# Optimization experiments

Hardware: AMD Instinct MI355X
Metric: run time of the kernel (lower is better)

Reference implementation:

```python
import jax, jax.numpy as jnp
import numpy as np

STATE_DIM, SKILL_DIM = 256, 64
HID = 1024
LAT = 128
B = 4096
TEMP = 1.0


def _init_linear(key, fan_in, fan_out):
    # torch nn.Linear default init: U(-1/sqrt(fan_in), 1/sqrt(fan_in))
    kw, kb = jax.random.split(key)
    bound = 1.0 / np.sqrt(fan_in)
    W = jax.random.uniform(kw, (fan_in, fan_out), jnp.float32, -bound, bound)
    b = jax.random.uniform(kb, (fan_out,), jnp.float32, -bound, bound)
    return W, b


def setup_inputs() -> dict:
    key = jax.random.key(0)
    ks = jax.random.split(key, 8)
    x = jax.random.normal(ks[0], (B, STATE_DIM), jnp.float32)
    y = jax.random.normal(ks[1], (B, SKILL_DIM), jnp.float32)
    sW1, sb1 = _init_linear(ks[2], STATE_DIM, HID)
    sW2, sb2 = _init_linear(ks[3], HID, HID)
    sW3, sb3 = _init_linear(ks[4], HID, LAT)
    kW1, kb1 = _init_linear(ks[5], SKILL_DIM, HID)
    kW2, kb2 = _init_linear(ks[6], HID, HID)
    kW3, kb3 = _init_linear(ks[7], HID, LAT)
    return {
        "x": x, "y": y,
        "sW1": sW1, "sb1": sb1, "sW2": sW2, "sb2": sb2, "sW3": sW3, "sb3": sb3,
        "kW1": kW1, "kb1": kb1, "kW2": kW2, "kb2": kb2, "kW3": kW3, "kb3": kb3,
    }


def _mlp(x, W1, b1, W2, b2, W3, b3):
    h = jax.nn.relu(x @ W1 + b1)
    h = jax.nn.relu(h @ W2 + b2)
    return h @ W3 + b3


def _l2norm(v, eps=1e-12):
    # matches F.normalize(dim=-1): v / max(||v||, eps)
    n = jnp.sqrt(jnp.sum(v * v, axis=-1, keepdims=True))
    return v / jnp.maximum(n, eps)


def reference(x, y, sW1, sb1, sW2, sb2, sW3, sb3, kW1, kb1, kW2, kb2, kW3, kb3):
    zx = _l2norm(_mlp(x, sW1, sb1, sW2, sb2, sW3, sb3))  # [B, LAT]
    zy = _l2norm(_mlp(y, kW1, kb1, kW2, kb2, kW3, kb3))  # [B, LAT]
    # sum(x[:,None,:]*y[None,:,:], -1) == zx @ zy.T (same math, no BxBxD blowup)
    scores = jnp.einsum('id,jd->ij', zx, zy) / TEMP       # [B, B]
    # InfoNCE lower bound: log(B) - CE(scores, arange(B)), reduction='none'
    logp = jax.nn.log_softmax(scores, axis=-1)
    nll = jnp.diagonal(logp)                               # = -CE per row
    mi = jnp.log(jnp.float32(scores.shape[0])) + nll       # [B]
    return scores, mi
```

## Files before the change

kernel.cpp:

```cpp
#include <hip/hip_runtime.h>
#include <hip/hip_bf16.h>
#include <math.h>

typedef __bf16 v8bf __attribute__((ext_vector_type(8)));
typedef float  v4f  __attribute__((ext_vector_type(4)));

#define GPTR(p) ((const __attribute__((address_space(1))) void*)(p))
#define LPTR(p) ((__attribute__((address_space(3))) void*)(p))

__global__ __launch_bounds__(256)
void cast_xy_k(const float* __restrict__ x, const float* __restrict__ y,
               __hip_bfloat16* __restrict__ xb, __hip_bfloat16* __restrict__ yb,
               int nx4, int ntot4) {
    int i = blockIdx.x * 256 + threadIdx.x;
    if (i >= ntot4) return;
    const float* src; __hip_bfloat16* dst; int j;
    if (i < nx4) { src = x; dst = xb; j = i; }
    else         { src = y; dst = yb; j = i - nx4; }
    float4 v = ((const float4*)src)[j];
    __hip_bfloat16 h[4] = {__float2bfloat16(v.x), __float2bfloat16(v.y),
                           __float2bfloat16(v.z), __float2bfloat16(v.w)};
    ((short4*)dst)[j] = *(short4*)h;
}

struct TransAll {
    const float* src[6];
    __hip_bfloat16* dst[6];
    int K[6], N[6];
};

__global__ __launch_bounds__(256)
void transpose_all_k(TransAll a) {
    int w = blockIdx.z;
    int K = a.K[w], N = a.N[w];
    int kt = blockIdx.x * 32, nt = blockIdx.y * 32;
    if (kt >= K || nt >= N) return;
    __shared__ float t[32][33];
    int tx = threadIdx.x & 31, ty = threadIdx.x >> 5;
    const float* W = a.src[w];
    __hip_bfloat16* Wt = a.dst[w];
#pragma unroll
    for (int i = 0; i < 4; ++i)
        t[ty + i * 8][tx] = W[(size_t)(kt + ty + i * 8) * N + nt + tx];
    __syncthreads();
#pragma unroll
    for (int i = 0; i < 4; ++i)
        Wt[(size_t)(nt + ty + i * 8) * K + kt + tx] =
            __float2bfloat16(t[tx][ty + i * 8]);
}

__device__ __forceinline__ void gemm_mainloop(
    const __hip_bfloat16* __restrict__ A, const __hip_bfloat16* __restrict__ Bt,
    int lda, int ldb, int kbeg, int kend, int bm, int bn,
    int wid, int lane, int wr, int wc,
    __hip_bfloat16* As, __hip_bfloat16* Bs, v4f acc[4][4]) {
    const int crow = lane >> 3;
    const int ccol = (lane & 7) * 8;
    for (int k0 = kbeg; k0 < kend; k0 += 64) {
#pragma unroll
        for (int i = 0; i < 4; ++i) {
            int c = wid * 4 + i;
            __builtin_amdgcn_global_load_lds(
                GPTR(A + (size_t)(bm + c * 8 + crow) * lda + k0 + ccol),
                LPTR(As + c * 512), 16, 0, 0);
            __builtin_amdgcn_global_load_lds(
                GPTR(Bt + (size_t)(bn + c * 8 + crow) * ldb + k0 + ccol),
                LPTR(Bs + c * 512), 16, 0, 0);
        }
        __syncthreads();
#pragma unroll
        for (int kk = 0; kk < 64; kk += 32) {
            v8bf a[4], b[4];
#pragma unroll
            for (int i = 0; i < 4; ++i) {
                a[i] = *(const v8bf*)&As[(wr * 64 + i * 16 + (lane & 15)) * 64 + kk + (lane >> 4) * 8];
                b[i] = *(const v8bf*)&Bs[(wc * 64 + i * 16 + (lane & 15)) * 64 + kk + (lane >> 4) * 8];
            }
#pragma unroll
            for (int i = 0; i < 4; ++i)
#pragma unroll
                for (int j = 0; j < 4; ++j)
                    acc[i][j] = __builtin_amdgcn_mfma_f32_16x16x32_bf16(
                        a[i], b[j], acc[i][j], 0, 0, 0);
        }
        __syncthreads();
    }
}

struct MlpArgs {
    const __hip_bfloat16* A[2];
    const __hip_bfloat16* B[2];
    const float* bias[2];
    __hip_bfloat16* C[2];
    int K[2];
};

__global__ __launch_bounds__(256)
void gemm_mlp_k(MlpArgs args) {
    __shared__ __align__(16) __hip_bfloat16 As[128 * 64], Bs[128 * 64];
    const int z = blockIdx.z;
    const int tid = threadIdx.x, wid = tid >> 6, lane = tid & 63;
    const int wr = wid >> 1, wc = wid & 1;
    const int bm = blockIdx.x * 128, bn = blockIdx.y * 128;
    const int K = args.K[z];
    v4f acc[4][4] = {};
    gemm_mainloop(args.A[z], args.B[z], K, K, 0, K, bm, bn, wid, lane, wr, wc,
                  As, Bs, acc);
    const float* bias = args.bias[z];
    __hip_bfloat16* C = args.C[z];
#pragma unroll
    for (int i = 0; i < 4; ++i) {
        int rowb = bm + wr * 64 + i * 16 + (lane >> 4) * 4;
#pragma unroll
        for (int j = 0; j < 4; ++j) {
            int col = bn + wc * 64 + j * 16 + (lane & 15);
            float bv = bias[col];
#pragma unroll
            for (int r = 0; r < 4; ++r) {
                float v = fmaxf(acc[i][j][r] + bv, 0.f);
                C[(size_t)(rowb + r) * 1024 + col] = __float2bfloat16(v);
            }
        }
    }
}

struct L3Args {
    const __hip_bfloat16* A[2];
    const __hip_bfloat16* B[2];
    float* part;
};

__global__ __launch_bounds__(256)
void gemm_l3_k(L3Args args) {
    __shared__ __align__(16) __hip_bfloat16 As[128 * 64], Bs[128 * 64];
    const int z = blockIdx.z, sp = blockIdx.y;
    const int tid = threadIdx.x, wid = tid >> 6, lane = tid & 63;
    const int wr = wid >> 1, wc = wid & 1;
    const int bm = blockIdx.x * 128;
    v4f acc[4][4] = {};
    gemm_mainloop(args.A[z], args.B[z], 1024, 1024, sp * 256, sp * 256 + 256,
                  bm, 0, wid, lane, wr, wc, As, Bs, acc);
    float* P = args.part + (size_t)(z * 4 + sp) * 4096 * 128;
#pragma unroll
    for (int i = 0; i < 4; ++i) {
        int rowb = bm + wr * 64 + i * 16 + (lane >> 4) * 4;
#pragma unroll
        for (int j = 0; j < 4; ++j) {
            int col = wc * 64 + j * 16 + (lane & 15);
#pragma unroll
            for (int r = 0; r < 4; ++r)
                P[(size_t)(rowb + r) * 128 + col] = acc[i][j][r];
        }
    }
}

__global__ __launch_bounds__(256)
void norm_k(const float* __restrict__ part, const float* __restrict__ sb3,
            const float* __restrict__ kb3,
            __hip_bfloat16* __restrict__ zxb, __hip_bfloat16* __restrict__ zyb) {
    int row  = blockIdx.x * 4 + (threadIdx.x >> 6);
    int lane = threadIdx.x & 63;
    int g = row >> 12;
    int r = row & 4095;
    const float* bias = g ? kb3 : sb3;
    float vx = bias[lane * 2], vy = bias[lane * 2 + 1];
#pragma unroll
    for (int s = 0; s < 4; ++s) {
        float2 p = *(const float2*)&part[((size_t)(g * 4 + s) * 4096 + r) * 128 + lane * 2];
        vx += p.x; vy += p.y;
    }
    float ss = vx * vx + vy * vy;
#pragma unroll
    for (int d = 32; d > 0; d >>= 1) ss += __shfl_xor(ss, d, 64);
    float inv = 1.0f / fmaxf(sqrtf(ss), 1e-12f);
    __hip_bfloat162 pr;
    pr.x = __float2bfloat16(vx * inv);
    pr.y = __float2bfloat16(vy * inv);
    __hip_bfloat16* out = g ? zyb : zxb;
    *(__hip_bfloat162*)&out[(size_t)r * 128 + lane * 2] = pr;
}

__global__ __launch_bounds__(256)
void gemm_scores_k(const __hip_bfloat16* __restrict__ zxb,
                   const __hip_bfloat16* __restrict__ zyb,
                   float* __restrict__ out, float* __restrict__ esum) {
    __shared__ __align__(16) __hip_bfloat16 As[128 * 64], Bs[128 * 64];
    __shared__ float rowsum[2][128];
    const int tid = threadIdx.x, wid = tid >> 6, lane = tid & 63;
    const int wr = wid >> 1, wc = wid & 1;
    const int bm = blockIdx.x * 128, bn = blockIdx.y * 128;
    v4f acc[4][4] = {};
    gemm_mainloop(zxb, zyb, 128, 128, 0, 128, bm, bn, wid, lane, wr, wc,
                  As, Bs, acc);
#pragma unroll
    for (int i = 0; i < 4; ++i) {
        int rowb = bm + wr * 64 + i * 16 + (lane >> 4) * 4;
#pragma unroll
        for (int r = 0; r < 4; ++r) {
            float s = 0.f;
#pragma unroll
            for (int j = 0; j < 4; ++j) {
                int col = bn + wc * 64 + j * 16 + (lane & 15);
                float v = acc[i][j][r];
                out[(size_t)(rowb + r) * 4096 + col] = v;
                s += __expf(v - 1.0f);
            }
#pragma unroll
            for (int m = 1; m < 16; m <<= 1) s += __shfl_xor(s, m, 64);
            if ((lane & 15) == 0)
                rowsum[wc][wr * 64 + i * 16 + (lane >> 4) * 4 + r] = s;
        }
    }
    __syncthreads();
    if (tid < 128)
        esum[(size_t)(bm + tid) * 32 + blockIdx.y] =
            rowsum[0][tid] + rowsum[1][tid];
}

__global__ __launch_bounds__(256)
void mi_k(const float* __restrict__ esum, const float* __restrict__ scores,
          float* __restrict__ mi) {
    int row = blockIdx.x * 256 + threadIdx.x;
    const float4* p = (const float4*)&esum[(size_t)row * 32];
    float s = 0.f;
#pragma unroll
    for (int i = 0; i < 8; ++i) { float4 v = p[i]; s += v.x + v.y + v.z + v.w; }
    float diag = scores[(size_t)row * 4096 + row];
    mi[row] = 8.317766166719343f + diag - 1.0f - logf(s);
}

extern "C" void kernel_launch(void* const* d_in, const int* in_sizes, int n_in,
                              void* d_out, int out_size, void* d_ws, size_t ws_size,
                              hipStream_t stream) {
    const float* x   = (const float*)d_in[0];
    const float* y   = (const float*)d_in[1];
    const float* sW1 = (const float*)d_in[2];
    const float* sb1 = (const float*)d_in[3];
    const float* sW2 = (const float*)d_in[4];
    const float* sb2 = (const float*)d_in[5];
    const float* sW3 = (const float*)d_in[6];
    const float* sb3 = (const float*)d_in[7];
    const float* kW1 = (const float*)d_in[8];
    const float* kb1 = (const float*)d_in[9];
    const float* kW2 = (const float*)d_in[10];
    const float* kb2 = (const float*)d_in[11];
    const float* kW3 = (const float*)d_in[12];
    const float* kb3 = (const float*)d_in[13];

    float* out = (float*)d_out;
    float* mi  = out + (size_t)4096 * 4096;

    char* ws = (char*)d_ws;
    auto alloc = [&](size_t bytes) {
        char* p = ws;
        ws += (bytes + 255) & ~(size_t)255;
        return p;
    };
    __hip_bfloat16* xb   = (__hip_bfloat16*)alloc((size_t)4096 * 256 * 2);
    __hip_bfloat16* yb   = (__hip_bfloat16*)alloc((size_t)4096 * 64 * 2);
    __hip_bfloat16* sW1t = (__hip_bfloat16*)alloc((size_t)1024 * 256 * 2);
    __hip_bfloat16* sW2t = (__hip_bfloat16*)alloc((size_t)1024 * 1024 * 2);
    __hip_bfloat16* sW3t = (__hip_bfloat16*)alloc((size_t)128 * 1024 * 2);
    __hip_bfloat16* kW1t = (__hip_bfloat16*)alloc((size_t)1024 * 64 * 2);
    __hip_bfloat16* kW2t = (__hip_bfloat16*)alloc((size_t)1024 * 1024 * 2);
    __hip_bfloat16* kW3t = (__hip_bfloat16*)alloc((size_t)128 * 1024 * 2);
    __hip_bfloat16* h1s  = (__hip_bfloat16*)alloc((size_t)4096 * 1024 * 2);
    __hip_bfloat16* h1k  = (__hip_bfloat16*)alloc((size_t)4096 * 1024 * 2);
    __hip_bfloat16* h2s  = (__hip_bfloat16*)alloc((size_t)4096 * 1024 * 2);
    __hip_bfloat16* h2k  = (__hip_bfloat16*)alloc((size_t)4096 * 1024 * 2);
    float*          part = (float*)alloc((size_t)8 * 4096 * 128 * 4);
    float*          es   = (float*)alloc((size_t)4096 * 32 * 4);
    __hip_bfloat16* zxb  = (__hip_bfloat16*)alloc((size_t)4096 * 128 * 2);
    __hip_bfloat16* zyb  = (__hip_bfloat16*)alloc((size_t)4096 * 128 * 2);

    int nx4 = 4096 * 256 / 4, ny4 = 4096 * 64 / 4;
    cast_xy_k<<<(nx4 + ny4 + 255) / 256, 256, 0, stream>>>(x, y, xb, yb, nx4, nx4 + ny4);

    TransAll ta;
    ta.src[0] = sW1; ta.dst[0] = sW1t; ta.K[0] = 256;  ta.N[0] = 1024;
    ta.src[1] = sW2; ta.dst[1] = sW2t; ta.K[1] = 1024; ta.N[1] = 1024;
    ta.src[2] = sW3; ta.dst[2] = sW3t; ta.K[2] = 1024; ta.N[2] = 128;
    ta.src[3] = kW1; ta.dst[3] = kW1t; ta.K[3] = 64;   ta.N[3] = 1024;
    ta.src[4] = kW2; ta.dst[4] = kW2t; ta.K[4] = 1024; ta.N[4] = 1024;
    ta.src[5] = kW3; ta.dst[5] = kW3t; ta.K[5] = 1024; ta.N[5] = 128;
    transpose_all_k<<<dim3(32, 32, 6), 256, 0, stream>>>(ta);

    MlpArgs l1;
    l1.A[0] = xb;  l1.B[0] = sW1t; l1.bias[0] = sb1; l1.C[0] = h1s; l1.K[0] = 256;
    l1.A[1] = yb;  l1.B[1] = kW1t; l1.bias[1] = kb1; l1.C[1] = h1k; l1.K[1] = 64;
    gemm_mlp_k<<<dim3(32, 8, 2), 256, 0, stream>>>(l1);

    MlpArgs l2;
    l2.A[0] = h1s; l2.B[0] = sW2t; l2.bias[0] = sb2; l2.C[0] = h2s; l2.K[0] = 1024;
    l2.A[1] = h1k; l2.B[1] = kW2t; l2.bias[1] = kb2; l2.C[1] = h2k; l2.K[1] = 1024;
    gemm_mlp_k<<<dim3(32, 8, 2), 256, 0, stream>>>(l2);

    L3Args l3;
    l3.A[0] = h2s; l3.B[0] = sW3t;
    l3.A[1] = h2k; l3.B[1] = kW3t;
    l3.part = part;
    gemm_l3_k<<<dim3(32, 4, 2), 256, 0, stream>>>(l3);

    norm_k<<<2048, 256, 0, stream>>>(part, sb3, kb3, zxb, zyb);

    gemm_scores_k<<<dim3(32, 32), 256, 0, stream>>>(zxb, zyb, out, es);

    mi_k<<<16, 256, 0, stream>>>(es, out, mi);
}
```

Baseline: 90.39 us.

## Fuse layer-3 GEMM with L2 normalization and merge cast/transpose prep kernels

Replaces the split-K layer-3 GEMM, which wrote fp32 partials, and the separate norm kernel with one kernel. It computes full-K 32x128 tiles, adds the bias, reduces the row sum of squares across waves in LDS, and writes normalized bf16 directly. This removes the partial-buffer round trip and one launch. The input cast and weight transposes are merged into a single launch, and the score stores become nontemporal. The cost is that the fused GEMM has only 256 blocks, each running a long K loop with no split, so its parallelism is lower.

Result: no change. 90.57 us (+0.2%).

```diff
diff --git a/kernel.cpp b/kernel.cpp
--- a/kernel.cpp
+++ b/kernel.cpp
@@ -8,37 +8,40 @@
 #define GPTR(p) ((const __attribute__((address_space(1))) void*)(p))
 #define LPTR(p) ((__attribute__((address_space(3))) void*)(p))
 
-__global__ __launch_bounds__(256)
-void cast_xy_k(const float* __restrict__ x, const float* __restrict__ y,
-               __hip_bfloat16* __restrict__ xb, __hip_bfloat16* __restrict__ yb,
-               int nx4, int ntot4) {
-    int i = blockIdx.x * 256 + threadIdx.x;
-    if (i >= ntot4) return;
-    const float* src; __hip_bfloat16* dst; int j;
-    if (i < nx4) { src = x; dst = xb; j = i; }
-    else         { src = y; dst = yb; j = i - nx4; }
-    float4 v = ((const float4*)src)[j];
-    __hip_bfloat16 h[4] = {__float2bfloat16(v.x), __float2bfloat16(v.y),
-                           __float2bfloat16(v.z), __float2bfloat16(v.w)};
-    ((short4*)dst)[j] = *(short4*)h;
-}
-
-struct TransAll {
-    const float* src[6];
-    __hip_bfloat16* dst[6];
+struct PrepArgs {
+    const float* x; const float* y;
+    __hip_bfloat16* xb; __hip_bfloat16* yb;
+    int nx4, ntot4;
+    const float* wsrc[6];
+    __hip_bfloat16* wdst[6];
     int K[6], N[6];
 };
 
 __global__ __launch_bounds__(256)
-void transpose_all_k(TransAll a) {
-    int w = blockIdx.z;
+void prep_k(PrepArgs a) {
+    const int tid = threadIdx.x, bx = blockIdx.x, z = blockIdx.z;
+    if (z == 0) {
+        int i = bx * 256 + tid;
+        if (i >= a.ntot4) return;
+        const float* src; __hip_bfloat16* dst; int j;
+        if (i < a.nx4) { src = a.x; dst = a.xb; j = i; }
+        else           { src = a.y; dst = a.yb; j = i - a.nx4; }
+        float4 v = ((const float4*)src)[j];
+        __hip_bfloat16 h[4] = {__float2bfloat16(v.x), __float2bfloat16(v.y),
+                               __float2bfloat16(v.z), __float2bfloat16(v.w)};
+        ((short4*)dst)[j] = *(short4*)h;
+        return;
+    }
+    int w = z - 1;
     int K = a.K[w], N = a.N[w];
-    int kt = blockIdx.x * 32, nt = blockIdx.y * 32;
-    if (kt >= K || nt >= N) return;
+    int tn = N >> 5;
+    int tt = (K >> 5) * tn;
+    if (bx >= tt) return;
+    int kt = (bx / tn) * 32, nt = (bx % tn) * 32;
     __shared__ float t[32][33];
-    int tx = threadIdx.x & 31, ty = threadIdx.x >> 5;
-    const float* W = a.src[w];
-    __hip_bfloat16* Wt = a.dst[w];
+    int tx = tid & 31, ty = tid >> 5;
+    const float* W = a.wsrc[w];
+    __hip_bfloat16* Wt = a.wdst[w];
 #pragma unroll
     for (int i = 0; i < 4; ++i)
         t[ty + i * 8][tx] = W[(size_t)(kt + ty + i * 8) * N + nt + tx];
@@ -124,60 +127,103 @@
     }
 }
 
-struct L3Args {
-    const __hip_bfloat16* A[2];
-    const __hip_bfloat16* B[2];
-    float* part;
-};
-
-__global__ __launch_bounds__(256)
-void gemm_l3_k(L3Args args) {
-    __shared__ __align__(16) __hip_bfloat16 As[128 * 64], Bs[128 * 64];
-    const int z = blockIdx.z, sp = blockIdx.y;
+__global__ __launch_bounds__(256)
+void gemm_l3norm_k(const __hip_bfloat16* __restrict__ As_g0,
+                   const __hip_bfloat16* __restrict__ As_g1,
+                   const __hip_bfloat16* __restrict__ Bt0,
+                   const __hip_bfloat16* __restrict__ Bt1,
+                   const float* __restrict__ sb3, const float* __restrict__ kb3,
+                   __hip_bfloat16* __restrict__ zxb,
+                   __hip_bfloat16* __restrict__ zyb) {
+    __shared__ __align__(16) __hip_bfloat16 As[32 * 64];
+    __shared__ __align__(16) __hip_bfloat16 Bs[128 * 64];
+    __shared__ float red[4][32];
+    const int z = blockIdx.y;
+    const __hip_bfloat16* A  = z ? As_g1 : As_g0;
+    const __hip_bfloat16* Bt = z ? Bt1 : Bt0;
+    const float* bias = z ? kb3 : sb3;
+    __hip_bfloat16* zout = z ? zyb : zxb;
+
     const int tid = threadIdx.x, wid = tid >> 6, lane = tid & 63;
-    const int wr = wid >> 1, wc = wid & 1;
-    const int bm = blockIdx.x * 128;
-    v4f acc[4][4] = {};
-    gemm_mainloop(args.A[z], args.B[z], 1024, 1024, sp * 256, sp * 256 + 256,
-                  bm, 0, wid, lane, wr, wc, As, Bs, acc);
-    float* P = args.part + (size_t)(z * 4 + sp) * 4096 * 128;
-#pragma unroll
-    for (int i = 0; i < 4; ++i) {
-        int rowb = bm + wr * 64 + i * 16 + (lane >> 4) * 4;
-#pragma unroll
-        for (int j = 0; j < 4; ++j) {
-            int col = wc * 64 + j * 16 + (lane & 15);
-#pragma unroll
-            for (int r = 0; r < 4; ++r)
-                P[(size_t)(rowb + r) * 128 + col] = acc[i][j][r];
-        }
-    }
-}
-
-__global__ __launch_bounds__(256)
-void norm_k(const float* __restrict__ part, const float* __restrict__ sb3,
-            const float* __restrict__ kb3,
-            __hip_bfloat16* __restrict__ zxb, __hip_bfloat16* __restrict__ zyb) {
-    int row  = blockIdx.x * 4 + (threadIdx.x >> 6);
-    int lane = threadIdx.x & 63;
-    int g = row >> 12;
-    int r = row & 4095;
-    const float* bias = g ? kb3 : sb3;
-    float vx = bias[lane * 2], vy = bias[lane * 2 + 1];
-#pragma unroll
-    for (int s = 0; s < 4; ++s) {
-        float2 p = *(const float2*)&part[((size_t)(g * 4 + s) * 4096 + r) * 128 + lane * 2];
-        vx += p.x; vy += p.y;
-    }
-    float ss = vx * vx + vy * vy;
-#pragma unroll
-    for (int d = 32; d > 0; d >>= 1) ss += __shfl_xor(ss, d, 64);
-    float inv = 1.0f / fmaxf(sqrtf(ss), 1e-12f);
-    __hip_bfloat162 pr;
-    pr.x = __float2bfloat16(vx * inv);
-    pr.y = __float2bfloat16(vy * inv);
-    __hip_bfloat16* out = g ? zyb : zxb;
-    *(__hip_bfloat162*)&out[(size_t)r * 128 + lane * 2] = pr;
+    const int bm = blockIdx.x * 32;
+    const int crow = lane >> 3, ccol = (lane & 7) * 8;
+
+    v4f acc[2][2] = {};
+    for (int k0 = 0; k0 < 1024; k0 += 64) {
+        __builtin_amdgcn_global_load_lds(
+            GPTR(A + (size_t)(bm + wid * 8 + crow) * 1024 + k0 + ccol),
+            LPTR(As + wid * 512), 16, 0, 0);
+#pragma unroll
+        for (int i = 0; i < 4; ++i) {
+            int c = wid * 4 + i;
+            __builtin_amdgcn_global_load_lds(
+                GPTR(Bt + (size_t)(c * 8 + crow) * 1024 + k0 + ccol),
+                LPTR(Bs + c * 512), 16, 0, 0);
+        }
+        __syncthreads();
+#pragma unroll
+        for (int kk = 0; kk < 64; kk += 32) {
+            v8bf a[2], b[2];
+#pragma unroll
+            for (int i = 0; i < 2; ++i)
+                a[i] = *(const v8bf*)&As[(i * 16 + (lane & 15)) * 64 + kk + (lane >> 4) * 8];
+#pragma unroll
+            for (int j = 0; j < 2; ++j)
+                b[j] = *(const v8bf*)&Bs[(wid * 32 + j * 16 + (lane & 15)) * 64 + kk + (lane >> 4) * 8];
+#pragma unroll
+            for (int i = 0; i < 2; ++i)
+#pragma unroll
+                for (int j = 0; j < 2; ++j)
+                    acc[i][j] = __builtin_amdgcn_mfma_f32_16x16x32_bf16(
+                        a[i], b[j], acc[i][j], 0, 0, 0);
+        }
+        __syncthreads();
+    }
+
+    float val[2][2][4];
+    float ssq[2][4];
+#pragma unroll
+    for (int i = 0; i < 2; ++i)
+#pragma unroll
+        for (int r = 0; r < 4; ++r) ssq[i][r] = 0.f;
+#pragma unroll
+    for (int i = 0; i < 2; ++i)
+#pragma unroll
+        for (int j = 0; j < 2; ++j) {
+            int col = wid * 32 + j * 16 + (lane & 15);
+            float bv = bias[col];
+#pragma unroll
+            for (int r = 0; r < 4; ++r) {
+                float v = acc[i][j][r] + bv;
+                val[i][j][r] = v;
+                ssq[i][r] += v * v;
+            }
+        }
+#pragma unroll
+    for (int i = 0; i < 2; ++i)
+#pragma unroll
+        for (int r = 0; r < 4; ++r) {
+#pragma unroll
+            for (int m = 1; m < 16; m <<= 1)
+                ssq[i][r] += __shfl_xor(ssq[i][r], m, 64);
+            if ((lane & 15) == 0)
+                red[wid][i * 16 + (lane >> 4) * 4 + r] = ssq[i][r];
+        }
+    __syncthreads();
+#pragma unroll
+    for (int i = 0; i < 2; ++i)
+#pragma unroll
+        for (int r = 0; r < 4; ++r) {
+            int row = i * 16 + (lane >> 4) * 4 + r;
+            float ss = red[0][row] + red[1][row] + red[2][row] + red[3][row];
+            float inv = 1.0f / fmaxf(sqrtf(ss), 1e-12f);
+#pragma unroll
+            for (int j = 0; j < 2; ++j) {
+                int col = wid * 32 + j * 16 + (lane & 15);
+                zout[(size_t)(bm + row) * 128 + col] =
+                    __float2bfloat16(val[i][j][r] * inv);
+            }
+        }
 }
 
 __global__ __launch_bounds__(256)
@@ -202,7 +248,7 @@
             for (int j = 0; j < 4; ++j) {
                 int col = bn + wc * 64 + j * 16 + (lane & 15);
                 float v = acc[i][j][r];
-                out[(size_t)(rowb + r) * 4096 + col] = v;
+                __builtin_nontemporal_store(v, &out[(size_t)(rowb + r) * 4096 + col]);
                 s += __expf(v - 1.0f);
             }
 #pragma unroll
@@ -268,22 +314,21 @@
     __hip_bfloat16* h1k  = (__hip_bfloat16*)alloc((size_t)4096 * 1024 * 2);
     __hip_bfloat16* h2s  = (__hip_bfloat16*)alloc((size_t)4096 * 1024 * 2);
     __hip_bfloat16* h2k  = (__hip_bfloat16*)alloc((size_t)4096 * 1024 * 2);
-    float*          part = (float*)alloc((size_t)8 * 4096 * 128 * 4);
     float*          es   = (float*)alloc((size_t)4096 * 32 * 4);
     __hip_bfloat16* zxb  = (__hip_bfloat16*)alloc((size_t)4096 * 128 * 2);
     __hip_bfloat16* zyb  = (__hip_bfloat16*)alloc((size_t)4096 * 128 * 2);
 
-    int nx4 = 4096 * 256 / 4, ny4 = 4096 * 64 / 4;
-    cast_xy_k<<<(nx4 + ny4 + 255) / 256, 256, 0, stream>>>(x, y, xb, yb, nx4, nx4 + ny4);
-
-    TransAll ta;
-    ta.src[0] = sW1; ta.dst[0] = sW1t; ta.K[0] = 256;  ta.N[0] = 1024;
-    ta.src[1] = sW2; ta.dst[1] = sW2t; ta.K[1] = 1024; ta.N[1] = 1024;
-    ta.src[2] = sW3; ta.dst[2] = sW3t; ta.K[2] = 1024; ta.N[2] = 128;
-    ta.src[3] = kW1; ta.dst[3] = kW1t; ta.K[3] = 64;   ta.N[3] = 1024;
-    ta.src[4] = kW2; ta.dst[4] = kW2t; ta.K[4] = 1024; ta.N[4] = 1024;
-    ta.src[5] = kW3; ta.dst[5] = kW3t; ta.K[5] = 1024; ta.N[5] = 128;
-    transpose_all_k<<<dim3(32, 32, 6), 256, 0, stream>>>(ta);
+    PrepArgs pa;
+    pa.x = x; pa.y = y; pa.xb = xb; pa.yb = yb;
+    pa.nx4 = 4096 * 256 / 4;
+    pa.ntot4 = pa.nx4 + 4096 * 64 / 4;
+    pa.wsrc[0] = sW1; pa.wdst[0] = sW1t; pa.K[0] = 256;  pa.N[0] = 1024;
+    pa.wsrc[1] = sW2; pa.wdst[1] = sW2t; pa.K[1] = 1024; pa.N[1] = 1024;
+    pa.wsrc[2] = sW3; pa.wdst[2] = sW3t; pa.K[2] = 1024; pa.N[2] = 128;
+    pa.wsrc[3] = kW1; pa.wdst[3] = kW1t; pa.K[3] = 64;   pa.N[3] = 1024;
+    pa.wsrc[4] = kW2; pa.wdst[4] = kW2t; pa.K[4] = 1024; pa.N[4] = 1024;
+    pa.wsrc[5] = kW3; pa.wdst[5] = kW3t; pa.K[5] = 1024; pa.N[5] = 128;
+    prep_k<<<dim3(1280, 1, 7), 256, 0, stream>>>(pa);
 
     MlpArgs l1;
     l1.A[0] = xb;  l1.B[0] = sW1t; l1.bias[0] = sb1; l1.C[0] = h1s; l1.K[0] = 256;
@@ -295,13 +340,8 @@
     l2.A[1] = h1k; l2.B[1] = kW2t; l2.bias[1] = kb2; l2.C[1] = h2k; l2.K[1] = 1024;
     gemm_mlp_k<<<dim3(32, 8, 2), 256, 0, stream>>>(l2);
 
-    L3Args l3;
-    l3.A[0] = h2s; l3.B[0] = sW3t;
-    l3.A[1] = h2k; l3.B[1] = kW3t;
-    l3.part = part;
-    gemm_l3_k<<<dim3(32, 4, 2), 256, 0, stream>>>(l3);
-
-    norm_k<<<2048, 256, 0, stream>>>(part, sb3, kb3, zxb, zyb);
+    gemm_l3norm_k<<<dim3(128, 2), 256, 0, stream>>>(
+        h2s, h2k, sW3t, kW3t, sb3, kb3, zxb, zyb);
 
     gemm_scores_k<<<dim3(32, 32), 256, 0, stream>>>(zxb, zyb, out, es);
 
```
